# Optimization experiments

Measured on AMD Instinct MI355X. Metric: run time of the kernel, lower is better.

Reference implementation:

```python
import jax, jax.numpy as jnp
import numpy as np

B, T, I, O = 64, 512, 512, 512
EPS = 1e-5


def setup_inputs() -> dict:
    key = jax.random.key(0)
    k1, k2 = jax.random.split(key)
    inpute = jax.random.normal(k1, (B, T, I), dtype=jnp.float32)
    W = jax.random.normal(k2, (I + O, 4 * O), dtype=jnp.float32) * 0.02
    b = jnp.zeros((4 * O,), dtype=jnp.float32)
    ln_w = jnp.ones((4, O), dtype=jnp.float32)
    ln_b = jnp.zeros((4, O), dtype=jnp.float32)
    init_hx = jnp.zeros((1, O), dtype=jnp.float32)
    init_cx = jnp.zeros((1, O), dtype=jnp.float32)
    return {"inpute": inpute, "W": W, "b": b, "ln_w": ln_w, "ln_b": ln_b,
            "init_hx": init_hx, "init_cx": init_cx}


def _cell(x_t, h, c, W, b, ln_w, ln_b):
    # x_t: [B, I], h/c: [B, O]
    comb = jnp.concatenate([x_t, h], axis=-1) @ W + b          # [B, 4O]
    comb = comb.reshape(-1, 4, O)                              # [B, 4, O]
    # LayerNorm over the last two dims (4, O), as nn.LayerNorm((4, osize))
    mu = comb.mean(axis=(-2, -1), keepdims=True)
    var = comb.var(axis=(-2, -1), keepdims=True)
    comb = (comb - mu) * jax.lax.rsqrt(var + EPS) * ln_w + ln_b
    gates = jax.nn.sigmoid(comb[:, :3])                        # ig, fg, og
    ig, fg, og = gates[:, 0], gates[:, 1], gates[:, 2]
    hidden = jnp.tanh(comb[:, 3])
    c = fg * c + ig * hidden
    h = og * c
    return h, c


def reference(inpute, W, b, ln_w, ln_b, init_hx, init_cx):
    bsize = inpute.shape[0]
    h0 = jnp.broadcast_to(init_hx, (bsize, O))
    c0 = jnp.broadcast_to(init_cx, (bsize, O))

    def step(carry, x_t):
        h, c = carry
        h, c = _cell(x_t, h, c, W, b, ln_w, ln_b)
        return (h, c), h

    xs = jnp.swapaxes(inpute, 0, 1)                            # [T, B, I]
    _, hs = jax.lax.scan(step, (h0, c0), xs)                   # [T, B, O]
    return jnp.swapaxes(hs, 0, 1)                              # [B, T, O]
```

## Files before the change

### kernel.cpp

```cpp
#include <hip/hip_runtime.h>
#include <hip/hip_bf16.h>

#define B_ 64
#define T_ 512
#define O_ 512
#define NWG 256
#define NTHR 256
#define EPSF 1e-5f

typedef __attribute__((ext_vector_type(8))) short short8v;
typedef __attribute__((ext_vector_type(4))) float f32x4;
typedef __attribute__((ext_vector_type(2))) float f32x2;
typedef unsigned short u16;
typedef unsigned int u32;
typedef unsigned long long u64;

__device__ __forceinline__ u16 f2bf(float f) {
    union { float f; u32 u; } v; v.f = f;
    u32 r = v.u + 0x7fffu + ((v.u >> 16) & 1u);
    return (u16)(r >> 16);
}
__device__ __forceinline__ float bf2f(u16 h) {
    union { u32 u; float f; } v; v.u = ((u32)h) << 16; return v.f;
}

__device__ __forceinline__ u32 ldg_sc1_u32(const u32* p) {
    return __hip_atomic_load(p, __ATOMIC_RELAXED, __HIP_MEMORY_SCOPE_AGENT);
}
__device__ __forceinline__ u64 ldg_sc1_u64(const void* p) {
    return __hip_atomic_load((const u64*)p, __ATOMIC_RELAXED, __HIP_MEMORY_SCOPE_AGENT);
}
__device__ __forceinline__ void stg_sc1_u32(u32* p, u32 v) {
    __hip_atomic_store(p, v, __ATOMIC_RELAXED, __HIP_MEMORY_SCOPE_AGENT);
}
__device__ __forceinline__ void stg_sc1_u64(u64* p, u64 v) {
    __hip_atomic_store(p, v, __ATOMIC_RELAXED, __HIP_MEMORY_SCOPE_AGENT);
}

__global__ void k_init_wt(const float* __restrict__ W, u16* __restrict__ wt) {
    __shared__ u16 tile[64][65];
    const int tk = (blockIdx.x >> 5) * 64;
    const int tn = (blockIdx.x & 31) * 64;
    const int r = threadIdx.x >> 6, c = threadIdx.x & 63;
#pragma unroll
    for (int i = 0; i < 16; ++i)
        tile[r + 4 * i][c] = f2bf(W[(size_t)(tk + r + 4 * i) * 2048 + tn + c]);
    __syncthreads();
#pragma unroll
    for (int i = 0; i < 16; ++i)
        wt[(size_t)(tn + r + 4 * i) * 1024 + tk + c] = tile[c][r + 4 * i];
}

__global__ void k_init_x(const float* __restrict__ x, u16* __restrict__ xbf) {
    size_t e = ((size_t)blockIdx.x * 256 + threadIdx.x) * 8;
    int b = (int)(e >> 18);
    int r = (int)(e & 262143);
    int t = r >> 9, k = r & 511;
    float4 u0 = *(const float4*)(x + e);
    float4 u1 = *(const float4*)(x + e + 4);
    short8v v;
    v[0] = (short)f2bf(u0.x); v[1] = (short)f2bf(u0.y);
    v[2] = (short)f2bf(u0.z); v[3] = (short)f2bf(u0.w);
    v[4] = (short)f2bf(u1.x); v[5] = (short)f2bf(u1.y);
    v[6] = (short)f2bf(u1.z); v[7] = (short)f2bf(u1.w);
    *(short8v*)(xbf + ((size_t)t * B_ + b) * 512 + k) = v;
}

__global__ void k_zero_flags(u32* grpfl) {
    int gid = blockIdx.x * 256 + threadIdx.x;
    if (gid < 512) stg_sc1_u32(grpfl + gid, 0u);
}

__global__ __launch_bounds__(NTHR, 1)
void k_persist(const u16* __restrict__ xbf, const u16* __restrict__ wt,
               const float* __restrict__ bias, const float* __restrict__ lnw,
               const float* __restrict__ lnb, const float* __restrict__ hx,
               const float* __restrict__ cx, u32* comb, float* statsp,
               u32* grpfl, float* __restrict__ out) {
    __shared__ u16 hT[4096];
    __shared__ f32x2 sp[4][8];
    __shared__ f32x2 sstat[8];

    const int tid = threadIdx.x, wgid = blockIdx.x;
    const int grp = wgid & 7, slot = wgid >> 3;
    const int w = tid >> 6, l = tid & 63;
    const int rl = l & 15, kg = l >> 4;
    const int arow = rl & 7;
    char* hTB = (char*)hT;
    u32* gf = grpfl + grp * 64;

    const int mycol = 512 * w + 16 * slot + rl;
    short8v bw[32];
#pragma unroll
    for (int kc = 0; kc < 32; ++kc)
        bw[kc] = *(const short8v*)(wt + (size_t)mycol * 1024 + kc * 32 + kg * 8);
    const float bcol = bias[mycol];

    const int po2 = tid * 2;
    float lwv[8], lbv[8];
#pragma unroll
    for (int g = 0; g < 4; ++g) {
        lwv[g * 2]     = lnw[g * 512 + po2];
        lwv[g * 2 + 1] = lnw[g * 512 + po2 + 1];
        lbv[g * 2]     = lnb[g * 512 + po2];
        lbv[g * 2 + 1] = lnb[g * 512 + po2 + 1];
    }
    float c16[16];
    {
        float c0 = cx[po2], c1 = cx[po2 + 1];
#pragma unroll
        for (int r = 0; r < 8; ++r) { c16[r * 2] = c0; c16[r * 2 + 1] = c1; }
        u32 hp = (u32)f2bf(hx[po2]) | ((u32)f2bf(hx[po2 + 1]) << 16);
#pragma unroll
        for (int r = 0; r < 8; ++r)
            *(u32*)(hTB + ((r * 1024 + po2 * 2) ^ (r << 4))) = hp;
    }
    __syncthreads();

    auto g_arrive = [&](u32 g) {
        asm volatile("s_waitcnt vmcnt(0)" ::: "memory");
        __syncthreads();
        if (tid == 0) stg_sc1_u32(gf + slot, g);
    };
    auto g_wait = [&](u32 g) {
        if (tid < 32) { while (!__all(ldg_sc1_u32(gf + tid) >= g)) {} }
        __syncthreads();
    };

    auto xgemm = [&](int t, f32x4& c0, f32x4& c1) {
        const u16* xr = xbf + ((size_t)t * B_ + grp * 8 + arow) * 512;
#pragma unroll
        for (int kc = 0; kc < 16; ++kc) {
            short8v a = *(const short8v*)(xr + kc * 32 + kg * 8);
            if (kc & 1) c1 = __builtin_amdgcn_mfma_f32_16x16x32_bf16(a, bw[kc], c1, 0, 0, 0);
            else        c0 = __builtin_amdgcn_mfma_f32_16x16x32_bf16(a, bw[kc], c0, 0, 0, 0);
        }
    };

    f32x4 xa0 = {0.f, 0.f, 0.f, 0.f}, xa1 = {0.f, 0.f, 0.f, 0.f};
    xgemm(0, xa0, xa1);

    for (int t = 0; t < T_; ++t) {
#pragma unroll
        for (int kc = 0; kc < 16; ++kc) {
            int byte = arow * 1024 + kc * 64 + kg * 16;
            short8v a = *(const short8v*)(hTB + (byte ^ (arow << 4)));
            if (kc & 1) xa1 = __builtin_amdgcn_mfma_f32_16x16x32_bf16(a, bw[16 + kc], xa1, 0, 0, 0);
            else        xa0 = __builtin_amdgcn_mfma_f32_16x16x32_bf16(a, bw[16 + kc], xa0, 0, 0, 0);
        }
        f32x4 acc = xa0 + xa1;

        const int cb = t & 1;
        u32*   combB = comb + (size_t)cb * (64 * 1024);
        float* statB = statsp + (size_t)cb * (64 * 32 * 2);

        float v4[4], vo[4], sj[4], qj[4];
#pragma unroll
        for (int j = 0; j < 4; ++j) {
            v4[j] = acc[j] + bcol;
            sj[j] = v4[j]; qj[j] = v4[j] * v4[j];
        }
#pragma unroll
        for (int j = 0; j < 4; ++j) vo[j] = __shfl_xor(v4[j], 1);
#pragma unroll
        for (int m = 1; m < 16; m <<= 1) {
#pragma unroll
            for (int j = 0; j < 4; ++j) {
                sj[j] += __shfl_xor(sj[j], m);
                qj[j] += __shfl_xor(qj[j], m);
            }
        }
        if (kg < 2) {
            if (!(rl & 1)) {
#pragma unroll
                for (int j = 0; j < 4; ++j) {
                    u32 pk = (u32)f2bf(v4[j]) | ((u32)f2bf(vo[j]) << 16);
                    stg_sc1_u32(combB + ((size_t)(grp * 8 + kg * 4 + j) * 1024
                                         + w * 256 + slot * 8 + (rl >> 1)), pk);
                }
            }
            if (rl == 0) {
#pragma unroll
                for (int j = 0; j < 4; ++j) sp[w][kg * 4 + j] = f32x2{sj[j], qj[j]};
            }
        }
        __syncthreads();
        if (tid < 8) {
            float S = sp[0][tid].x + sp[1][tid].x + sp[2][tid].x + sp[3][tid].x;
            float Q = sp[0][tid].y + sp[1][tid].y + sp[2][tid].y + sp[3][tid].y;
            union { float f[2]; u64 q; } uu; uu.f[0] = S; uu.f[1] = Q;
            stg_sc1_u64((u64*)(statB + ((size_t)(grp * 8 + tid) * 32 + slot) * 2), uu.q);
        }

        g_arrive(t + 1);
        if (t + 1 < T_) {
            xa0 = f32x4{0.f, 0.f, 0.f, 0.f}; xa1 = f32x4{0.f, 0.f, 0.f, 0.f};
            xgemm(t + 1, xa0, xa1);
        }
        g_wait(t + 1);

        u32 cgf[8][4];
#pragma unroll
        for (int r = 0; r < 8; ++r) {
#pragma unroll
            for (int g = 0; g < 4; ++g)
                cgf[r][g] = ldg_sc1_u32(combB + ((size_t)(grp * 8 + r) * 1024
                                                 + g * 256 + tid));
        }
        {
            union { u64 q; float f[2]; } uu;
            uu.q = ldg_sc1_u64(statB + ((size_t)(grp * 8 + (tid >> 5)) * 32 + (tid & 31)) * 2);
            float s = uu.f[0], q = uu.f[1];
#pragma unroll
            for (int m = 1; m < 32; m <<= 1) {
                s += __shfl_xor(s, m);
                q += __shfl_xor(q, m);
            }
            if ((tid & 31) == 0) sstat[tid >> 5] = f32x2{s, q};
        }
        __syncthreads();

#pragma unroll
        for (int r = 0; r < 8; ++r) {
            float S = sstat[r].x, Q = sstat[r].y;
            float mu = S * (1.0f / 2048.0f);
            float var = Q * (1.0f / 2048.0f) - mu * mu;
            float rstd = rsqrtf(var + EPSF);
            float hh[2];
#pragma unroll
            for (int i = 0; i < 2; ++i) {
                float cv0 = bf2f((u16)(cgf[r][0] >> (16 * i)));
                float cv1 = bf2f((u16)(cgf[r][1] >> (16 * i)));
                float cv2 = bf2f((u16)(cgf[r][2] >> (16 * i)));
                float cv3 = bf2f((u16)(cgf[r][3] >> (16 * i)));
                float g0 = (cv0 - mu) * rstd * lwv[0 + i] + lbv[0 + i];
                float g1 = (cv1 - mu) * rstd * lwv[2 + i] + lbv[2 + i];
                float g2 = (cv2 - mu) * rstd * lwv[4 + i] + lbv[4 + i];
                float g3 = (cv3 - mu) * rstd * lwv[6 + i] + lbv[6 + i];
                float ig = 1.f / (1.f + __expf(-g0));
                float fg = 1.f / (1.f + __expf(-g1));
                float og = 1.f / (1.f + __expf(-g2));
                float e2 = __expf(-2.f * fabsf(g3));
                float th = copysignf((1.f - e2) / (1.f + e2), g3);
                float cc = fg * c16[r * 2 + i] + ig * th;
                c16[r * 2 + i] = cc;
                hh[i] = og * cc;
            }
            u32 hp = (u32)f2bf(hh[0]) | ((u32)f2bf(hh[1]) << 16);
            *(u32*)(hTB + ((r * 1024 + po2 * 2) ^ (r << 4))) = hp;
            if (slot == 0) {
                f32x2 ho{hh[0], hh[1]};
                __builtin_nontemporal_store(ho,
                    (f32x2*)(out + (size_t)(grp * 8 + r) * (T_ * O_) + (size_t)t * O_ + po2));
            }
        }
        __syncthreads();
    }
}

extern "C" void kernel_launch(void* const* d_in, const int* in_sizes, int n_in,
                              void* d_out, int out_size, void* d_ws, size_t ws_size,
                              hipStream_t stream) {
    const float* x    = (const float*)d_in[0];
    const float* W    = (const float*)d_in[1];
    const float* bias = (const float*)d_in[2];
    const float* lnw  = (const float*)d_in[3];
    const float* lnb  = (const float*)d_in[4];
    const float* hx   = (const float*)d_in[5];
    const float* cx   = (const float*)d_in[6];
    float* out = (float*)d_out;

    char* ws = (char*)d_ws;
    u16*   wt     = (u16*)ws;
    u16*   xbf    = (u16*)(ws + 4194304);
    u32*   comb   = (u32*)(ws + 37748736);
    float* statsp = (float*)(ws + 38273024);
    u32*   grpfl  = (u32*)(ws + 38305792);

    k_init_wt<<<512, 256, 0, stream>>>(W, wt);
    k_init_x<<<8192, 256, 0, stream>>>(x, xbf);
    k_zero_flags<<<2, 256, 0, stream>>>(grpfl);
    k_persist<<<NWG, NTHR, 0, stream>>>(xbf, wt, bias, lnw, lnb, hx, cx,
                                        comb, statsp, grpfl, out);
}
```

Before: 3.669 ms.

## Compute LayerNorm stats from gathered gates and use per-producer flag waits

Drops the separate stats exchange buffer. Each workgroup now rebuilds the LayerNorm sum and sum-of-squares from the bf16 gate values it already gathers, which removes one global store/load round per step and the pre-arrive block reduction. The gate buffer is relaid out so each thread reads its 8 rows with vectorized dwordx4 loads. Each thread spin-waits only on the flag of the producer whose data it consumes, instead of a wave-wide all-flags check followed by a barrier. In exchange, stats are computed from bf16-rounded values, which changes numerics slightly, and the final reduction needs more shuffles.

```diff
diff --git a/kernel.cpp b/kernel.cpp
--- a/kernel.cpp
+++ b/kernel.cpp
@@ -11,6 +11,7 @@
 typedef __attribute__((ext_vector_type(8))) short short8v;
 typedef __attribute__((ext_vector_type(4))) float f32x4;
 typedef __attribute__((ext_vector_type(2))) float f32x2;
+typedef __attribute__((ext_vector_type(4))) unsigned int u32x4;
 typedef unsigned short u16;
 typedef unsigned int u32;
 typedef unsigned long long u64;
@@ -27,13 +28,7 @@
 __device__ __forceinline__ u32 ldg_sc1_u32(const u32* p) {
     return __hip_atomic_load(p, __ATOMIC_RELAXED, __HIP_MEMORY_SCOPE_AGENT);
 }
-__device__ __forceinline__ u64 ldg_sc1_u64(const void* p) {
-    return __hip_atomic_load((const u64*)p, __ATOMIC_RELAXED, __HIP_MEMORY_SCOPE_AGENT);
-}
 __device__ __forceinline__ void stg_sc1_u32(u32* p, u32 v) {
-    __hip_atomic_store(p, v, __ATOMIC_RELAXED, __HIP_MEMORY_SCOPE_AGENT);
-}
-__device__ __forceinline__ void stg_sc1_u64(u64* p, u64 v) {
     __hip_atomic_store(p, v, __ATOMIC_RELAXED, __HIP_MEMORY_SCOPE_AGENT);
 }
 
@@ -75,8 +70,8 @@
 void k_persist(const u16* __restrict__ xbf, const u16* __restrict__ wt,
                const float* __restrict__ bias, const float* __restrict__ lnw,
                const float* __restrict__ lnb, const float* __restrict__ hx,
-               const float* __restrict__ cx, u32* comb, float* statsp,
-               u32* grpfl, float* __restrict__ out) {
+               const float* __restrict__ cx, u32* comb, u32* grpfl,
+               float* __restrict__ out) {
     __shared__ u16 hT[4096];
     __shared__ f32x2 sp[4][8];
     __shared__ f32x2 sstat[8];
@@ -88,6 +83,7 @@
     const int arow = rl & 7;
     char* hTB = (char*)hT;
     u32* gf = grpfl + grp * 64;
+    const int myprod = tid >> 3;
 
     const int mycol = 512 * w + 16 * slot + rl;
     short8v bw[32];
@@ -117,16 +113,6 @@
     }
     __syncthreads();
 
-    auto g_arrive = [&](u32 g) {
-        asm volatile("s_waitcnt vmcnt(0)" ::: "memory");
-        __syncthreads();
-        if (tid == 0) stg_sc1_u32(gf + slot, g);
-    };
-    auto g_wait = [&](u32 g) {
-        if (tid < 32) { while (!__all(ldg_sc1_u32(gf + tid) >= g)) {} }
-        __syncthreads();
-    };
-
     auto xgemm = [&](int t, f32x4& c0, f32x4& c1) {
         const u16* xr = xbf + ((size_t)t * B_ + grp * 8 + arow) * 512;
 #pragma unroll
@@ -151,73 +137,72 @@
         f32x4 acc = xa0 + xa1;
 
         const int cb = t & 1;
-        u32*   combB = comb + (size_t)cb * (64 * 1024);
-        float* statB = statsp + (size_t)cb * (64 * 32 * 2);
-
-        float v4[4], vo[4], sj[4], qj[4];
-#pragma unroll
-        for (int j = 0; j < 4; ++j) {
-            v4[j] = acc[j] + bcol;
-            sj[j] = v4[j]; qj[j] = v4[j] * v4[j];
-        }
+        u32* combB = comb + (size_t)cb * 65536 + (size_t)grp * 8192;
+
+        float v4[4], vo[4];
+#pragma unroll
+        for (int j = 0; j < 4; ++j) v4[j] = acc[j] + bcol;
 #pragma unroll
         for (int j = 0; j < 4; ++j) vo[j] = __shfl_xor(v4[j], 1);
-#pragma unroll
-        for (int m = 1; m < 16; m <<= 1) {
+        if (kg < 2 && !(rl & 1)) {
+            int pair = slot * 8 + (rl >> 1);
 #pragma unroll
             for (int j = 0; j < 4; ++j) {
-                sj[j] += __shfl_xor(sj[j], m);
-                qj[j] += __shfl_xor(qj[j], m);
-            }
-        }
-        if (kg < 2) {
-            if (!(rl & 1)) {
-#pragma unroll
-                for (int j = 0; j < 4; ++j) {
-                    u32 pk = (u32)f2bf(v4[j]) | ((u32)f2bf(vo[j]) << 16);
-                    stg_sc1_u32(combB + ((size_t)(grp * 8 + kg * 4 + j) * 1024
-                                         + w * 256 + slot * 8 + (rl >> 1)), pk);
-                }
-            }
-            if (rl == 0) {
-#pragma unroll
-                for (int j = 0; j < 4; ++j) sp[w][kg * 4 + j] = f32x2{sj[j], qj[j]};
-            }
-        }
-        __syncthreads();
-        if (tid < 8) {
-            float S = sp[0][tid].x + sp[1][tid].x + sp[2][tid].x + sp[3][tid].x;
-            float Q = sp[0][tid].y + sp[1][tid].y + sp[2][tid].y + sp[3][tid].y;
-            union { float f[2]; u64 q; } uu; uu.f[0] = S; uu.f[1] = Q;
-            stg_sc1_u64((u64*)(statB + ((size_t)(grp * 8 + tid) * 32 + slot) * 2), uu.q);
-        }
-
-        g_arrive(t + 1);
+                u32 pk = (u32)f2bf(v4[j]) | ((u32)f2bf(vo[j]) << 16);
+                stg_sc1_u32(combB + pair * 32 + (kg * 4 + j) * 4 + w, pk);
+            }
+        }
+        asm volatile("s_waitcnt vmcnt(0)" ::: "memory");
+        __syncthreads();
+        if (tid == 0) stg_sc1_u32(gf + slot, (u32)(t + 1));
+
         if (t + 1 < T_) {
             xa0 = f32x4{0.f, 0.f, 0.f, 0.f}; xa1 = f32x4{0.f, 0.f, 0.f, 0.f};
             xgemm(t + 1, xa0, xa1);
         }
-        g_wait(t + 1);
-
-        u32 cgf[8][4];
+
+        while (ldg_sc1_u32(gf + myprod) < (u32)(t + 1)) {}
+        u32x4 cg[8];
+        {
+            const u32* gbase = combB + tid * 32;
+#pragma unroll
+            for (int r = 0; r < 8; ++r)
+                asm volatile("global_load_dwordx4 %0, %1, off sc1"
+                             : "=v"(cg[r]) : "v"(gbase + r * 4) : "memory");
+            asm volatile("s_waitcnt vmcnt(0)" ::: "memory");
+            __builtin_amdgcn_sched_barrier(0);
+        }
+
+        float s8[8], q8[8];
 #pragma unroll
         for (int r = 0; r < 8; ++r) {
-#pragma unroll
-            for (int g = 0; g < 4; ++g)
-                cgf[r][g] = ldg_sc1_u32(combB + ((size_t)(grp * 8 + r) * 1024
-                                                 + g * 256 + tid));
-        }
-        {
-            union { u64 q; float f[2]; } uu;
-            uu.q = ldg_sc1_u64(statB + ((size_t)(grp * 8 + (tid >> 5)) * 32 + (tid & 31)) * 2);
-            float s = uu.f[0], q = uu.f[1];
-#pragma unroll
-            for (int m = 1; m < 32; m <<= 1) {
-                s += __shfl_xor(s, m);
-                q += __shfl_xor(q, m);
-            }
-            if ((tid & 31) == 0) sstat[tid >> 5] = f32x2{s, q};
-        }
+            float s = 0.f, q = 0.f;
+#pragma unroll
+            for (int g = 0; g < 4; ++g) {
+#pragma unroll
+                for (int i = 0; i < 2; ++i) {
+                    float v = bf2f((u16)(cg[r][g] >> (16 * i)));
+                    s += v; q += v * v;
+                }
+            }
+            s8[r] = s; q8[r] = q;
+        }
+#pragma unroll
+        for (int m = 1; m < 64; m <<= 1) {
+#pragma unroll
+            for (int r = 0; r < 8; ++r) {
+                s8[r] += __shfl_xor(s8[r], m);
+                q8[r] += __shfl_xor(q8[r], m);
+            }
+        }
+        if (l == 0) {
+#pragma unroll
+            for (int r = 0; r < 8; ++r) sp[w][r] = f32x2{s8[r], q8[r]};
+        }
+        __syncthreads();
+        if (tid < 8)
+            sstat[tid] = f32x2{sp[0][tid].x + sp[1][tid].x + sp[2][tid].x + sp[3][tid].x,
+                               sp[0][tid].y + sp[1][tid].y + sp[2][tid].y + sp[3][tid].y};
         __syncthreads();
 
 #pragma unroll
@@ -229,10 +214,10 @@
             float hh[2];
 #pragma unroll
             for (int i = 0; i < 2; ++i) {
-                float cv0 = bf2f((u16)(cgf[r][0] >> (16 * i)));
-                float cv1 = bf2f((u16)(cgf[r][1] >> (16 * i)));
-                float cv2 = bf2f((u16)(cgf[r][2] >> (16 * i)));
-                float cv3 = bf2f((u16)(cgf[r][3] >> (16 * i)));
+                float cv0 = bf2f((u16)(cg[r][0] >> (16 * i)));
+                float cv1 = bf2f((u16)(cg[r][1] >> (16 * i)));
+                float cv2 = bf2f((u16)(cg[r][2] >> (16 * i)));
+                float cv3 = bf2f((u16)(cg[r][3] >> (16 * i)));
                 float g0 = (cv0 - mu) * rstd * lwv[0 + i] + lbv[0 + i];
                 float g1 = (cv1 - mu) * rstd * lwv[2 + i] + lbv[2 + i];
                 float g2 = (cv2 - mu) * rstd * lwv[4 + i] + lbv[4 + i];
@@ -271,15 +256,14 @@
     float* out = (float*)d_out;
 
     char* ws = (char*)d_ws;
-    u16*   wt     = (u16*)ws;
-    u16*   xbf    = (u16*)(ws + 4194304);
-    u32*   comb   = (u32*)(ws + 37748736);
-    float* statsp = (float*)(ws + 38273024);
-    u32*   grpfl  = (u32*)(ws + 38305792);
+    u16*   wt    = (u16*)ws;
+    u16*   xbf   = (u16*)(ws + 4194304);
+    u32*   comb  = (u32*)(ws + 37748736);
+    u32*   grpfl = (u32*)(ws + 38273024);
 
     k_init_wt<<<512, 256, 0, stream>>>(W, wt);
     k_init_x<<<8192, 256, 0, stream>>>(x, xbf);
     k_zero_flags<<<2, 256, 0, stream>>>(grpfl);
     k_persist<<<NWG, NTHR, 0, stream>>>(xbf, wt, bias, lnw, lnb, hx, cx,
-                                        comb, statsp, grpfl, out);
-}
+                                        comb, grpfl, out);
+}
```

New measurement: 5.076 ms. +38.3%, slower.
